# Optimization experiments

Measured on AMD Instinct MI355X. Metric: run time of the kernel, lower is better.

Reference implementation:

```python
import jax, jax.numpy as jnp
import numpy as np

B, T, F, U = 64, 512, 32, 64
EPS = 1e-3  # keras LayerNormalization default epsilon


def _ln(x, g, b):
    m = jnp.mean(x, axis=-1, keepdims=True)
    v = jnp.var(x, axis=-1, keepdims=True)
    return (x - m) / jnp.sqrt(v + EPS) * g + b


def setup_inputs() -> dict:
    key = jax.random.key(0)
    ks = jax.random.split(key, 24)
    s = 0.05
    inp = {
        "x": jax.random.normal(ks[0], (B, T, F), dtype=jnp.float32),
        # per-feature GRNs, stacked over F (each sub-net has independent params)
        "W1": jax.random.normal(ks[1], (F, U), jnp.float32) * s,   # dense_1 (1->U)
        "b1": jnp.zeros((F, U), jnp.float32),
        "W2": jax.random.normal(ks[2], (F, U, U), jnp.float32) * s,  # dense_2 (U->U)
        "b2": jnp.zeros((F, U), jnp.float32),
        "Wg1": jax.random.normal(ks[3], (F, U, U), jnp.float32) * s,  # GLU linear
        "bg1": jnp.zeros((F, U), jnp.float32),
        "Wg2": jax.random.normal(ks[4], (F, U, U), jnp.float32) * s,  # GLU gate
        "bg2": jnp.zeros((F, U), jnp.float32),
        "Wp": jax.random.normal(ks[5], (F, U), jnp.float32) * s,   # project (1->U)
        "bp": jnp.zeros((F, U), jnp.float32),
        "gamma": jnp.ones((F, U), jnp.float32),
        "beta": jnp.zeros((F, U), jnp.float32),
        # weights GRN (F -> F, no projection since in_dim == units == F)
        "w1w": jax.random.normal(ks[6], (F, F), jnp.float32) * s,
        "b1w": jnp.zeros((F,), jnp.float32),
        "w2w": jax.random.normal(ks[7], (F, F), jnp.float32) * s,
        "b2w": jnp.zeros((F,), jnp.float32),
        "wg1w": jax.random.normal(ks[8], (F, F), jnp.float32) * s,
        "bg1w": jnp.zeros((F,), jnp.float32),
        "wg2w": jax.random.normal(ks[9], (F, F), jnp.float32) * s,
        "bg2w": jnp.zeros((F,), jnp.float32),
        "gammaw": jnp.ones((F,), jnp.float32),
        "betaw": jnp.zeros((F,), jnp.float32),
    }
    return inp


def reference(x, W1, b1, W2, b2, Wg1, bg1, Wg2, bg2, Wp, bp, gamma, beta,
              w1w, b1w, w2w, b2w, wg1w, bg1w, wg2w, bg2w, gammaw, betaw):
    # ---- variable weights GRN on flattened features (input dim F == units F, no projection) ----
    h = jax.nn.elu(jnp.einsum('btf,fg->btg', x, w1w) + b1w)
    h = jnp.einsum('btf,fg->btg', h, w2w) + b2w
    g = (jnp.einsum('btf,fg->btg', h, wg1w) + bg1w) * jax.nn.sigmoid(
        jnp.einsum('btf,fg->btg', h, wg2w) + bg2w)
    w = _ln(g + x, gammaw, betaw)
    w = jax.nn.softmax(w, axis=-1)  # [B,T,F]

    # ---- per-feature GRNs, batched over F (scalar input per feature) ----
    xe = x[..., None]                                   # [B,T,F,1]
    res = xe * Wp + bp                                  # project residual [B,T,F,U]
    h = jax.nn.elu(xe * W1 + b1)                        # dense_1 [B,T,F,U]
    h = jnp.einsum('btfu,fuv->btfv', h, W2) + b2        # dense_2
    g = (jnp.einsum('btfu,fuv->btfv', h, Wg1) + bg1) * jax.nn.sigmoid(
        jnp.einsum('btfu,fuv->btfv', h, Wg2) + bg2)     # GLU
    y = _ln(g + res, gamma, beta)                       # [B,T,F,U]

    out = jnp.einsum('btfu,btf->btu', y, w)             # softmax-weighted sum over features
    return out, w
```

## Files before the change

### kernel.cpp

```cpp
#include <hip/hip_runtime.h>
#include <hip/hip_bf16.h>


typedef float f4      __attribute__((ext_vector_type(4)));
typedef float f32x4   __attribute__((ext_vector_type(4)));
typedef short bf16x8  __attribute__((ext_vector_type(8)));
typedef unsigned short u16x4 __attribute__((ext_vector_type(4)));
typedef unsigned short u16x8 __attribute__((ext_vector_type(8)));

#define N_ROWS 32768
#define F_DIM  32
#define U_DIM  64
#define RPB    16
#define NTHR   256
#define NBLK   (N_ROWS / RPB)
#define LOG2E  1.4426950408889634f

#define PHA_FRAG 49152
#define VECT_BYTE_OFF 794624

#define X_OFF   0
#define WT_OFF  2304
#define VA_OFF  3584
#define VST_OFF 4352
#define SMEM_BYTES 17408

__device__ __forceinline__ unsigned short bfu(float x) {
  union { __hip_bfloat16 h; unsigned short u; } c;
  c.h = __float2bfloat16(x);
  return c.u;
}
__device__ __forceinline__ float bf2f(unsigned short u) {
  union { float f; unsigned v; } c; c.v = ((unsigned)u) << 16; return c.f;
}

__global__ __launch_bounds__(256) void vsn_prep(
    const float* __restrict__ W2,  const float* __restrict__ Wg1, const float* __restrict__ Wg2,
    const float* __restrict__ W1,  const float* __restrict__ b1,  const float* __restrict__ b2,
    const float* __restrict__ bg1, const float* __restrict__ bg2,
    const float* __restrict__ Wp,  const float* __restrict__ bp,
    const float* __restrict__ gamma_, const float* __restrict__ beta_,
    const float* __restrict__ w1w, const float* __restrict__ w2w,
    const float* __restrict__ wg1w, const float* __restrict__ wg2w,
    unsigned short* __restrict__ wtg, float* __restrict__ vect)
{
  const int t = threadIdx.x, blk = blockIdx.x;
  if (blk < 192) {
    const int m = blk >> 6;
    const int f = (blk >> 1) & 31;
    const int half = blk & 1;
    const float* src = (m == 0) ? W2 : (m == 1) ? Wg1 : Wg2;
    src += f * 4096;
    const float sc = (m == 2) ? -LOG2E : 1.0f;
    const int c  = half * 256 + t;
    const int nt = c >> 7;
    const int rr = c & 127;
    const int kt = rr >> 6;
    const int ln = rr & 63;
    const int g  = ln >> 4, lrr = ln & 15;
    const int uo = lrr + 16 * nt;
    u16x8 tmp;
    if (m == 0) {
      #pragma unroll
      for (int j = 0; j < 8; ++j)
        tmp[j] = bfu(src[(8 * g + 32 * kt + j) * 64 + uo]);
    } else {
      #pragma unroll
      for (int j = 0; j < 8; ++j)
        tmp[j] = bfu(src[(4 * g + (j & 3) + 16 * (j >> 2) + 32 * kt) * 64 + uo] * sc);
    }
    *(u16x8*)(wtg + ((size_t)(m * 32 + f) * 512 + c) * 8) = tmp;
  } else if (blk < 194) {
    const int h = blk - 192;
    for (int i = h * 1024 + t; i < (h + 1) * 1024; i += 256) {
      const int f = i >> 6, u = i & 63;
      float* vf = vect + f * 576;
      vf[u]       = W1[i];
      vf[64 + u]  = b1[i];
      vf[128 + u] = b2[i];
      vf[192 + u] = bg1[i];
      vf[256 + u] = bg2[i] * (-LOG2E);
      vf[320 + u] = Wp[i];
      vf[384 + u] = bp[i];
      vf[448 + u] = gamma_[i];
      vf[512 + u] = beta_[i];
    }
  } else {
    #pragma unroll
    for (int cc = 0; cc < 2; ++cc) {
      const int q = t + cc * 256;
      const int mat = q >> 7;
      const int nt  = (q >> 6) & 1;
      const int ln  = q & 63;
      const int lr  = ln & 15, lg = ln >> 4;
      const float* src = (mat == 0) ? w1w : (mat == 1) ? w2w : (mat == 2) ? wg1w : wg2w;
      const float sc = (mat == 3) ? -LOG2E : 1.0f;
      u16x8 tmp;
      if (mat == 0) {
        #pragma unroll
        for (int j = 0; j < 8; ++j)
          tmp[j] = bfu(src[(8 * lg + j) * 32 + lr + 16 * nt]);
      } else {
        #pragma unroll
        for (int j = 0; j < 8; ++j)
          tmp[j] = bfu(src[(4 * lg + (j & 3) + 16 * (j >> 2)) * 32 + lr + 16 * nt] * sc);
      }
      *(u16x8*)(wtg + ((size_t)PHA_FRAG + q) * 8) = tmp;
    }
  }
}

__global__ __launch_bounds__(NTHR, 4) void vsn_main(
    const float* __restrict__ x,
    const unsigned short* __restrict__ wtg,
    const float* __restrict__ vect,
    const float* __restrict__ b1w, const float* __restrict__ b2w,
    const float* __restrict__ bg1w, const float* __restrict__ bg2w,
    const float* __restrict__ gammaw, const float* __restrict__ betaw,
    float* __restrict__ out, float* __restrict__ wout)
{
  __shared__ __align__(16) char smem[SMEM_BYTES];
  const int t  = threadIdx.x;
  const int r0 = blockIdx.x * RPB;

  float* xt  = (float*)(smem + X_OFF);
  unsigned short* wtlb = (unsigned short*)(smem + WT_OFF);
  float* vAl = (float*)(smem + VA_OFF);
  float* vstf = (float*)(smem + VST_OFF);

  const int wid  = t >> 6;
  const int lane = t & 63;
  const int lr   = lane & 15;
  const int lg   = lane >> 4;
  const int fbase = wid * 8;

  if (t < 128) {
    f4 v = ((const f4*)(x + (size_t)r0 * F_DIM))[t];
    *((f4*)(xt + (t >> 3) * 36 + ((t & 7) << 2))) = v;
  }
  if (t < 48) {
    int m = t >> 3, off = (t & 7) << 2;
    const float* src = (m==0)?b1w:(m==1)?b2w:(m==2)?bg1w:(m==3)?bg2w:(m==4)?gammaw:betaw;
    f4 v = *((const f4*)(src + off));
    if (m == 3) { v[0]*=-LOG2E; v[1]*=-LOG2E; v[2]*=-LOG2E; v[3]*=-LOG2E; }
    *(f4*)(vAl + m * 32 + off) = v;
  }

  const f4* vect4 = (const f4*)vect;
  f4 rv0 = vect4[fbase * 144 + lane];
  f4 rv1 = vect4[fbase * 144 + 64 + lane];
  f4 rv2 = {};
  if (lane < 16) rv2 = vect4[fbase * 144 + 128 + lane];

  __syncthreads();

  f4* vst4 = ((f4*)vstf) + wid * 144;
  float* vsc = vstf + wid * 576;
  vst4[lane] = rv0; vst4[64 + lane] = rv1;
  if (lane < 16) vst4[128 + lane] = rv2;

  {
    const bf16x8* pf = ((const bf16x8*)wtg) + PHA_FRAG;

    f4 xa0 = *(const f4*)(xt + lr * 36 + 8 * lg);
    f4 xa1 = *(const f4*)(xt + lr * 36 + 8 * lg + 4);
    bf16x8 xb;
    #pragma unroll
    for (int j = 0; j < 4; ++j) { xb[j] = (short)bfu(xa0[j]); xb[4 + j] = (short)bfu(xa1[j]); }

    f32x4 c1a[2];
    #pragma unroll
    for (int nt = 0; nt < 2; ++nt)
      c1a[nt] = __builtin_amdgcn_mfma_f32_16x16x32_bf16(
          pf[(0 * 2 + nt) * 64 + lane], xb,
          *(const f32x4*)(vAl + 4 * lg + 16 * nt), 0, 0, 0);
    bf16x8 hf;
    #pragma unroll
    for (int nt = 0; nt < 2; ++nt)
      #pragma unroll
      for (int rg = 0; rg < 4; ++rg) {
        float h = c1a[nt][rg];
        hf[nt * 4 + rg] = (short)bfu(h > 0.f ? h : (__expf(h) - 1.f));
      }

    f32x4 c2a[2];
    #pragma unroll
    for (int nt = 0; nt < 2; ++nt)
      c2a[nt] = __builtin_amdgcn_mfma_f32_16x16x32_bf16(
          pf[(1 * 2 + nt) * 64 + lane], hf,
          *(const f32x4*)(vAl + 32 + 4 * lg + 16 * nt), 0, 0, 0);
    bf16x8 h2f;
    #pragma unroll
    for (int nt = 0; nt < 2; ++nt)
      #pragma unroll
      for (int rg = 0; rg < 4; ++rg)
        h2f[nt * 4 + rg] = (short)bfu(c2a[nt][rg]);

    f32x4 cga[2], cgb[2];
    #pragma unroll
    for (int nt = 0; nt < 2; ++nt) {
      cga[nt] = __builtin_amdgcn_mfma_f32_16x16x32_bf16(
          pf[(2 * 2 + nt) * 64 + lane], h2f,
          *(const f32x4*)(vAl + 64 + 4 * lg + 16 * nt), 0, 0, 0);
      cgb[nt] = __builtin_amdgcn_mfma_f32_16x16x32_bf16(
          pf[(3 * 2 + nt) * 64 + lane], h2f,
          *(const f32x4*)(vAl + 96 + 4 * lg + 16 * nt), 0, 0, 0);
    }
    float zv[8];
    float s1 = 0.f, s2 = 0.f;
    #pragma unroll
    for (int nt = 0; nt < 2; ++nt)
      #pragma unroll
      for (int rg = 0; rg < 4; ++rg) {
        const int g = 4 * lg + rg + 16 * nt;
        float sg = __builtin_amdgcn_rcpf(1.f + __builtin_amdgcn_exp2f(cgb[nt][rg]));
        float z = cga[nt][rg] * sg + xt[lr * 36 + g];
        zv[nt * 4 + rg] = z;
        s1 += z; s2 += z * z;
      }
    s1 += __shfl_xor(s1, 16, 64); s1 += __shfl_xor(s1, 32, 64);
    s2 += __shfl_xor(s2, 16, 64); s2 += __shfl_xor(s2, 32, 64);
    const float mA = s1 * 0.03125f;
    const float vA = s2 * 0.03125f - mA * mA;
    const float rsA = __builtin_amdgcn_rsqf(vA + 1e-3f);
    float yv[8], mx = -1e30f;
    #pragma unroll
    for (int nt = 0; nt < 2; ++nt)
      #pragma unroll
      for (int rg = 0; rg < 4; ++rg) {
        const int g = 4 * lg + rg + 16 * nt;
        float y = (zv[nt * 4 + rg] - mA) * rsA * vAl[128 + g] + vAl[160 + g];
        yv[nt * 4 + rg] = y;
        mx = fmaxf(mx, y);
      }
    mx = fmaxf(mx, __shfl_xor(mx, 16, 64));
    mx = fmaxf(mx, __shfl_xor(mx, 32, 64));
    float ev[8], es = 0.f;
    #pragma unroll
    for (int j = 0; j < 8; ++j) { ev[j] = __expf(yv[j] - mx); es += ev[j]; }
    es += __shfl_xor(es, 16, 64); es += __shfl_xor(es, 32, 64);
    const float inv = __builtin_amdgcn_rcpf(es);
    #pragma unroll
    for (int nt = 0; nt < 2; ++nt)
      #pragma unroll
      for (int rg = 0; rg < 4; ++rg) {
        const int g = 4 * lg + rg + 16 * nt;
        wtlb[lr * 40 + g] = bfu(ev[nt * 4 + rg] * inv);
      }
    if (t < 128) {
      const int row = t >> 3, c4 = (t & 7) << 2;
      u16x4 wq = *(const u16x4*)(wtlb + row * 40 + c4);
      f4 wo = { bf2f(wq[0]), bf2f(wq[1]), bf2f(wq[2]), bf2f(wq[3]) };
      *(f4*)(wout + (size_t)(r0 + row) * 32 + c4) = wo;
    }
  }

  const bf16x8* wf = (const bf16x8*)wtg;

  f32x4 acc[4];
  #pragma unroll
  for (int nt = 0; nt < 4; ++nt) acc[nt] = (f32x4){0.f, 0.f, 0.f, 0.f};

  for (int i = 0; i < 8; ++i) {
    const int f = fbase + i;

    const int base0 = (0 * 32 + f) * 512 + lane;
    bf16x8 w2f[8];
    #pragma unroll
    for (int nt = 0; nt < 4; ++nt)
      #pragma unroll
      for (int kt = 0; kt < 2; ++kt)
        w2f[nt * 2 + kt] = wf[base0 + nt * 128 + kt * 64];

    const float s_ = xt[lr * 36 + f];
    bf16x8 afr[2];
    #pragma unroll
    for (int kt = 0; kt < 2; ++kt) {
      const int u0 = 8 * lg + 32 * kt;
      f4 wa  = *(const f4*)(vsc + u0);
      f4 wb_ = *(const f4*)(vsc + u0 + 4);
      f4 ba  = *(const f4*)(vsc + 64 + u0);
      f4 bb_ = *(const f4*)(vsc + 64 + u0 + 4);
      bf16x8 af;
      #pragma unroll
      for (int j = 0; j < 4; ++j) {
        float h = s_ * wa[j] + ba[j];
        h = h > 0.f ? h : (__expf(h) - 1.f);
        af[j] = (short)bfu(h);
      }
      #pragma unroll
      for (int j = 0; j < 4; ++j) {
        float h = s_ * wb_[j] + bb_[j];
        h = h > 0.f ? h : (__expf(h) - 1.f);
        af[4 + j] = (short)bfu(h);
      }
      afr[kt] = af;
    }

    f32x4 c1[4];
    #pragma unroll
    for (int nt = 0; nt < 4; ++nt) {
      c1[nt] = *(const f32x4*)(vsc + 128 + 4 * lg + 16 * nt);
      #pragma unroll
      for (int kt = 0; kt < 2; ++kt)
        c1[nt] = __builtin_amdgcn_mfma_f32_16x16x32_bf16(w2f[nt * 2 + kt], afr[kt], c1[nt], 0, 0, 0);
    }

    bf16x8 a2[2];
    #pragma unroll
    for (int kt = 0; kt < 2; ++kt) {
      bf16x8 af;
      #pragma unroll
      for (int j = 0; j < 8; ++j)
        af[j] = (short)bfu(c1[(j >> 2) + 2 * kt][j & 3]);
      a2[kt] = af;
    }

    const int base1 = (1 * 32 + f) * 512 + lane;
    bf16x8 bfa[8];
    #pragma unroll
    for (int nt = 0; nt < 4; ++nt)
      #pragma unroll
      for (int kt = 0; kt < 2; ++kt)
        bfa[nt * 2 + kt] = wf[base1 + nt * 128 + kt * 64];
    f32x4 ca[4], cb[4];
    #pragma unroll
    for (int nt = 0; nt < 4; ++nt) {
      ca[nt] = *(const f32x4*)(vsc + 192 + 16 * nt + 4 * lg);
      #pragma unroll
      for (int kt = 0; kt < 2; ++kt)
        ca[nt] = __builtin_amdgcn_mfma_f32_16x16x32_bf16(bfa[nt * 2 + kt], a2[kt], ca[nt], 0, 0, 0);
    }

    const int base2 = (2 * 32 + f) * 512 + lane;
    bf16x8 bfb[8];
    #pragma unroll
    for (int nt = 0; nt < 4; ++nt)
      #pragma unroll
      for (int kt = 0; kt < 2; ++kt)
        bfb[nt * 2 + kt] = wf[base2 + nt * 128 + kt * 64];
    #pragma unroll
    for (int nt = 0; nt < 4; ++nt) {
      cb[nt] = *(const f32x4*)(vsc + 256 + 16 * nt + 4 * lg);
      #pragma unroll
      for (int kt = 0; kt < 2; ++kt)
        cb[nt] = __builtin_amdgcn_mfma_f32_16x16x32_bf16(bfb[nt * 2 + kt], a2[kt], cb[nt], 0, 0, 0);
    }

    if (i < 7) {
      rv0 = vect4[(f + 1) * 144 + lane];
      rv1 = vect4[(f + 1) * 144 + 64 + lane];
      if (lane < 16) rv2 = vect4[(f + 1) * 144 + 128 + lane];
    }

    const float wr_ = bf2f(wtlb[lr * 40 + f]);
    float zf[4][4];
    float s1 = 0.f, s2 = 0.f;
    #pragma unroll
    for (int nt = 0; nt < 4; ++nt) {
      f4 wp4 = *(const f4*)(vsc + 320 + 16 * nt + 4 * lg);
      f4 bp4 = *(const f4*)(vsc + 384 + 16 * nt + 4 * lg);
      #pragma unroll
      for (int rg = 0; rg < 4; ++rg) {
        float sg = __builtin_amdgcn_rcpf(1.f + __builtin_amdgcn_exp2f(cb[nt][rg]));
        float z = ca[nt][rg] * sg + (s_ * wp4[rg] + bp4[rg]);
        zf[nt][rg] = z;
        s1 += z;
        s2 += z * z;
      }
    }
    s1 += __shfl_xor(s1, 16, 64); s1 += __shfl_xor(s1, 32, 64);
    s2 += __shfl_xor(s2, 16, 64); s2 += __shfl_xor(s2, 32, 64);
    const float mn = s1 * 0.015625f;
    const float var = s2 * 0.015625f - mn * mn;
    const float rs = __builtin_amdgcn_rsqf(var + 1e-3f);
    const float rswr = rs * wr_;
    const float nc2 = -mn * rswr;
    #pragma unroll
    for (int nt = 0; nt < 4; ++nt) {
      f4 g4 = *(const f4*)(vsc + 448 + 16 * nt + 4 * lg);
      f4 b4 = *(const f4*)(vsc + 512 + 16 * nt + 4 * lg);
      #pragma unroll
      for (int rg = 0; rg < 4; ++rg)
        acc[nt][rg] += g4[rg] * (rswr * zf[nt][rg] + nc2) + b4[rg] * wr_;
    }

    if (i < 7) {
      vst4[lane] = rv0; vst4[64 + lane] = rv1;
      if (lane < 16) vst4[128 + lane] = rv2;
    }
  }

  __syncthreads();
  float* cmb = (float*)smem;
  #pragma unroll
  for (int nt = 0; nt < 4; ++nt)
    *(f4*)(cmb + wid * 1088 + lr * 68 + 16 * nt + 4 * lg) = acc[nt];
  __syncthreads();
  {
    const int row = t >> 4, u4 = (t & 15) << 2;
    const float* cp = cmb + row * 68 + u4;
    f4 o = *(const f4*)(cp) + *(const f4*)(cp + 1088) +
           *(const f4*)(cp + 2176) + *(const f4*)(cp + 3264);
    *(f4*)(out + (size_t)(r0 + row) * U_DIM + u4) = o;
  }
}

extern "C" void kernel_launch(void* const* d_in, const int* in_sizes, int n_in,
                              void* d_out, int out_size, void* d_ws, size_t ws_size,
                              hipStream_t stream)
{
  (void)in_sizes; (void)n_in; (void)out_size; (void)ws_size;
  const float* x    = (const float*)d_in[0];
  const float* W1   = (const float*)d_in[1];
  const float* b1   = (const float*)d_in[2];
  const float* W2   = (const float*)d_in[3];
  const float* b2   = (const float*)d_in[4];
  const float* Wg1  = (const float*)d_in[5];
  const float* bg1  = (const float*)d_in[6];
  const float* Wg2  = (const float*)d_in[7];
  const float* bg2  = (const float*)d_in[8];
  const float* Wp   = (const float*)d_in[9];
  const float* bp   = (const float*)d_in[10];
  const float* gm   = (const float*)d_in[11];
  const float* bt   = (const float*)d_in[12];
  const float* w1w  = (const float*)d_in[13];
  const float* b1w  = (const float*)d_in[14];
  const float* w2w  = (const float*)d_in[15];
  const float* b2w  = (const float*)d_in[16];
  const float* wg1w = (const float*)d_in[17];
  const float* bg1w = (const float*)d_in[18];
  const float* wg2w = (const float*)d_in[19];
  const float* bg2w = (const float*)d_in[20];
  const float* gmw  = (const float*)d_in[21];
  const float* btw  = (const float*)d_in[22];

  unsigned short* wtg = (unsigned short*)d_ws;
  float* vect = (float*)((char*)d_ws + VECT_BYTE_OFF);

  float* out  = (float*)d_out;
  float* wout = out + (size_t)N_ROWS * U_DIM;

  vsn_prep<<<195, 256, 0, stream>>>(W2, Wg1, Wg2, W1, b1, b2, bg1, bg2, Wp, bp, gm, bt,
                                    w1w, w2w, wg1w, wg2w, wtg, vect);
  vsn_main<<<NBLK, NTHR, 0, stream>>>(x, wtg, vect,
                                      b1w, b2w, bg1w, bg2w, gmw, btw, out, wout);
}
```

Baseline: 178.5 us.

## Reorder GLU matmuls, pack LN inputs to bf16, raise occupancy to 5 waves

```diff
diff --git a/kernel.cpp b/kernel.cpp
--- a/kernel.cpp
+++ b/kernel.cpp
@@ -32,6 +32,12 @@
 }
 __device__ __forceinline__ float bf2f(unsigned short u) {
   union { float f; unsigned v; } c; c.v = ((unsigned)u) << 16; return c.f;
+}
+__device__ __forceinline__ float bflo(unsigned p) {
+  union { float f; unsigned v; } c; c.v = p << 16; return c.f;
+}
+__device__ __forceinline__ float bfhi(unsigned p) {
+  union { float f; unsigned v; } c; c.v = p & 0xffff0000u; return c.f;
 }
 
 __global__ __launch_bounds__(256) void vsn_prep(
@@ -110,7 +116,7 @@
   }
 }
 
-__global__ __launch_bounds__(NTHR, 4) void vsn_main(
+__global__ __launch_bounds__(NTHR, 5) void vsn_main(
     const float* __restrict__ x,
     const unsigned short* __restrict__ wtg,
     const float* __restrict__ vect,
@@ -149,8 +155,7 @@
   const f4* vect4 = (const f4*)vect;
   f4 rv0 = vect4[fbase * 144 + lane];
   f4 rv1 = vect4[fbase * 144 + 64 + lane];
-  f4 rv2 = {};
-  if (lane < 16) rv2 = vect4[fbase * 144 + 128 + lane];
+  f4 rv2 = vect4[fbase * 144 + 128 + (lane & 15)];
 
   __syncthreads();
 
@@ -298,6 +303,7 @@
     }
 
     f32x4 c1[4];
+    __builtin_amdgcn_s_setprio(1);
     #pragma unroll
     for (int nt = 0; nt < 4; ++nt) {
       c1[nt] = *(const f32x4*)(vsc + 128 + 4 * lg + 16 * nt);
@@ -305,6 +311,7 @@
       for (int kt = 0; kt < 2; ++kt)
         c1[nt] = __builtin_amdgcn_mfma_f32_16x16x32_bf16(w2f[nt * 2 + kt], afr[kt], c1[nt], 0, 0, 0);
     }
+    __builtin_amdgcn_s_setprio(0);
 
     bf16x8 a2[2];
     #pragma unroll
@@ -316,59 +323,65 @@
       a2[kt] = af;
     }
 
-    const int base1 = (1 * 32 + f) * 512 + lane;
-    bf16x8 bfa[8];
-    #pragma unroll
-    for (int nt = 0; nt < 4; ++nt)
-      #pragma unroll
-      for (int kt = 0; kt < 2; ++kt)
-        bfa[nt * 2 + kt] = wf[base1 + nt * 128 + kt * 64];
-    f32x4 ca[4], cb[4];
-    #pragma unroll
-    for (int nt = 0; nt < 4; ++nt) {
-      ca[nt] = *(const f32x4*)(vsc + 192 + 16 * nt + 4 * lg);
-      #pragma unroll
-      for (int kt = 0; kt < 2; ++kt)
-        ca[nt] = __builtin_amdgcn_mfma_f32_16x16x32_bf16(bfa[nt * 2 + kt], a2[kt], ca[nt], 0, 0, 0);
-    }
-
-    const int base2 = (2 * 32 + f) * 512 + lane;
-    bf16x8 bfb[8];
-    #pragma unroll
-    for (int nt = 0; nt < 4; ++nt)
-      #pragma unroll
-      for (int kt = 0; kt < 2; ++kt)
-        bfb[nt * 2 + kt] = wf[base2 + nt * 128 + kt * 64];
-    #pragma unroll
-    for (int nt = 0; nt < 4; ++nt) {
-      cb[nt] = *(const f32x4*)(vsc + 256 + 16 * nt + 4 * lg);
-      #pragma unroll
-      for (int kt = 0; kt < 2; ++kt)
-        cb[nt] = __builtin_amdgcn_mfma_f32_16x16x32_bf16(bfb[nt * 2 + kt], a2[kt], cb[nt], 0, 0, 0);
-    }
-
     if (i < 7) {
       rv0 = vect4[(f + 1) * 144 + lane];
       rv1 = vect4[(f + 1) * 144 + 64 + lane];
-      if (lane < 16) rv2 = vect4[(f + 1) * 144 + 128 + lane];
-    }
+      rv2 = vect4[(f + 1) * 144 + 128 + (lane & 15)];
+    }
+
+    const int base2 = (2 * 32 + f) * 512 + lane;
+    bf16x8 bfb[8];
+    #pragma unroll
+    for (int nt = 0; nt < 4; ++nt)
+      #pragma unroll
+      for (int kt = 0; kt < 2; ++kt)
+        bfb[nt * 2 + kt] = wf[base2 + nt * 128 + kt * 64];
+    float gate[4][4];
+    __builtin_amdgcn_s_setprio(1);
+    #pragma unroll
+    for (int nt = 0; nt < 4; ++nt) {
+      f32x4 cb = *(const f32x4*)(vsc + 256 + 16 * nt + 4 * lg);
+      #pragma unroll
+      for (int kt = 0; kt < 2; ++kt)
+        cb = __builtin_amdgcn_mfma_f32_16x16x32_bf16(bfb[nt * 2 + kt], a2[kt], cb, 0, 0, 0);
+      #pragma unroll
+      for (int rg = 0; rg < 4; ++rg)
+        gate[nt][rg] = __builtin_amdgcn_rcpf(1.f + __builtin_amdgcn_exp2f(cb[rg]));
+    }
+    __builtin_amdgcn_s_setprio(0);
+
+    const int base1 = (1 * 32 + f) * 512 + lane;
+    bf16x8 bfa[8];
+    #pragma unroll
+    for (int nt = 0; nt < 4; ++nt)
+      #pragma unroll
+      for (int kt = 0; kt < 2; ++kt)
+        bfa[nt * 2 + kt] = wf[base1 + nt * 128 + kt * 64];
 
     const float wr_ = bf2f(wtlb[lr * 40 + f]);
-    float zf[4][4];
+    unsigned zp[8];
     float s1 = 0.f, s2 = 0.f;
+    __builtin_amdgcn_s_setprio(1);
     #pragma unroll
     for (int nt = 0; nt < 4; ++nt) {
+      f32x4 ca = *(const f32x4*)(vsc + 192 + 16 * nt + 4 * lg);
+      #pragma unroll
+      for (int kt = 0; kt < 2; ++kt)
+        ca = __builtin_amdgcn_mfma_f32_16x16x32_bf16(bfa[nt * 2 + kt], a2[kt], ca, 0, 0, 0);
       f4 wp4 = *(const f4*)(vsc + 320 + 16 * nt + 4 * lg);
       f4 bp4 = *(const f4*)(vsc + 384 + 16 * nt + 4 * lg);
+      float zq[4];
       #pragma unroll
       for (int rg = 0; rg < 4; ++rg) {
-        float sg = __builtin_amdgcn_rcpf(1.f + __builtin_amdgcn_exp2f(cb[nt][rg]));
-        float z = ca[nt][rg] * sg + (s_ * wp4[rg] + bp4[rg]);
-        zf[nt][rg] = z;
+        float z = ca[rg] * gate[nt][rg] + (s_ * wp4[rg] + bp4[rg]);
+        zq[rg] = z;
         s1 += z;
         s2 += z * z;
       }
-    }
+      zp[2 * nt]     = (unsigned)bfu(zq[0]) | ((unsigned)bfu(zq[1]) << 16);
+      zp[2 * nt + 1] = (unsigned)bfu(zq[2]) | ((unsigned)bfu(zq[3]) << 16);
+    }
+    __builtin_amdgcn_s_setprio(0);
     s1 += __shfl_xor(s1, 16, 64); s1 += __shfl_xor(s1, 32, 64);
     s2 += __shfl_xor(s2, 16, 64); s2 += __shfl_xor(s2, 32, 64);
     const float mn = s1 * 0.015625f;
@@ -380,9 +393,12 @@
     for (int nt = 0; nt < 4; ++nt) {
       f4 g4 = *(const f4*)(vsc + 448 + 16 * nt + 4 * lg);
       f4 b4 = *(const f4*)(vsc + 512 + 16 * nt + 4 * lg);
-      #pragma unroll
-      for (int rg = 0; rg < 4; ++rg)
-        acc[nt][rg] += g4[rg] * (rswr * zf[nt][rg] + nc2) + b4[rg] * wr_;
+      const unsigned pA = zp[2 * nt], pB = zp[2 * nt + 1];
+      const float z0 = bflo(pA), z1 = bfhi(pA), z2 = bflo(pB), z3 = bfhi(pB);
+      acc[nt][0] += g4[0] * (rswr * z0 + nc2) + b4[0] * wr_;
+      acc[nt][1] += g4[1] * (rswr * z1 + nc2) + b4[1] * wr_;
+      acc[nt][2] += g4[2] * (rswr * z2 + nc2) + b4[2] * wr_;
+      acc[nt][3] += g4[3] * (rswr * z3 + nc2) + b4[3] * wr_;
     }
 
     if (i < 7) {
```

New measurement: 226.8 us. +27.0%, slower.
